# Kernel optimization log

Hardware: AMD Instinct MI355X
Metric: run time of the kernel (lower is better)

## Reference

```python
import jax, jax.numpy as jnp
import numpy as np
from jax import lax

NUM_MASK_PARAMS = 67  # 66 weights (64 feat + 2 coord channels) + 1 bias
NUM_GEN_PARAMS = 134


def _coord_maps(h, w, dtype):
    yy = jnp.broadcast_to(jnp.linspace(-1.0, 1.0, h, dtype=dtype)[:, None], (h, w))
    xx = jnp.broadcast_to(jnp.linspace(-1.0, 1.0, w, dtype=dtype)[None, :], (h, w))
    return xx, yy


def _dynamic_head(x_cat, p):
    # x_cat: [66, H, W]; p: [num_ins, 67] -> [num_ins, H, W]
    w = p[:, :NUM_MASK_PARAMS - 1]
    b = p[:, NUM_MASK_PARAMS - 1]
    return jnp.einsum('ic,chw->ihw', w, x_cat) + b[:, None, None]


def setup_inputs() -> dict:
    key = jax.random.key(0)
    ks = jax.random.split(key, 10)
    C, HM, WM, HH, WH, MB, HID = 256, 272, 480, 136, 240, 64, 64
    rn = lambda k, s, sc=1.0: jax.random.normal(k, s, dtype=jnp.float32) * sc
    return {
        'out0': rn(ks[0], (1, C, HM, WM)),
        'out1': rn(ks[1], (1, C, HH, WH)),
        'hm_w': rn(ks[2], (1, C), 0.05),
        'hm_b': jnp.zeros((1,), jnp.float32),
        'params_w': rn(ks[3], (NUM_GEN_PARAMS, C), 0.05),
        'params_b': rn(ks[4], (NUM_GEN_PARAMS,), 0.05),
        'mb_w': rn(ks[5], (MB, C, 3, 3), 0.05),
        'mb_b': jnp.zeros((MB,), jnp.float32),
        'mlp_w1': rn(ks[6], (HM, HID), 0.05),
        'mlp_b1': jnp.zeros((HID,), jnp.float32),
        'mlp_w2': rn(ks[7], (HID, 2), 0.05),
        'mlp_b2': jnp.zeros((2,), jnp.float32),
        'num_ins': 4,
    }


def reference(out0, out1, hm_w, hm_b, params_w, params_b, mb_w, mb_b,
              mlp_w1, mlp_b1, mlp_w2, mlp_b2, num_ins):
    h_mask, w_mask = out0.shape[2], out0.shape[3]
    h_hm, w_hm = out1.shape[2], out1.shape[3]

    # ctnet head: 1x1 convs on the stride-16 feature
    hm = jnp.einsum('kc,bchw->bkhw', hm_w, out1) + hm_b[None, :, None, None]
    params = jnp.einsum('kc,bchw->bkhw', params_w, out1) + params_b[None, :, None, None]
    hm = jnp.clip(jax.nn.sigmoid(hm), 1e-4, 1.0 - 1e-4)  # [1,1,h_hm,w_hm]
    # [1,134,h,w] -> [h*w, 134]
    params_flat = jnp.transpose(params[0], (1, 2, 0)).reshape(-1, NUM_GEN_PARAMS)

    # 3x3 maxpool NMS (stride 1, pad 1), keep only local peaks
    hmax = lax.reduce_window(hm, -jnp.inf, lax.max, (1, 1, 3, 3), (1, 1, 1, 1),
                             [(0, 0), (0, 0), (1, 1), (1, 1)])
    keep = (hmax == hm).astype(hm.dtype)
    heat_nms = (hm * keep).reshape(-1)

    scores, inds = lax.top_k(heat_nms, num_ins)

    # mask branch: 3x3 conv + relu on the stride-8 feature
    mask_branch = lax.conv_general_dilated(out0, mb_w, (1, 1), 'SAME',
                                           dimension_numbers=('NCHW', 'OIHW', 'NCHW'))
    mask_branch = jax.nn.relu(mask_branch + mb_b[None, :, None, None])  # [1,64,H,W]

    xx, yy = _coord_maps(h_mask, w_mask, mask_branch.dtype)
    x_cat = jnp.concatenate([mask_branch[0], xx[None], yy[None]], axis=0)  # [66,H,W]

    gen_params = params_flat[inds]  # [num_ins, 134]
    masks0 = _dynamic_head(x_cat, gen_params[:, :NUM_MASK_PARAMS])   # [num_ins,H,W]
    regs0 = _dynamic_head(x_cat, gen_params[:, NUM_MASK_PARAMS:])    # [num_ins,H,W]

    # row-wise vertical-range MLP over h_mask
    feat_range = jnp.transpose(masks0, (0, 2, 1))  # [num_ins, w_mask, h_mask]
    h1 = jax.nn.relu(feat_range @ mlp_w1 + mlp_b1)
    feat_range = h1 @ mlp_w2 + mlp_b2  # [num_ins, w_mask, 2]

    return scores, inds, regs0, masks0, feat_range
```

## Files before the change

kernel.cpp:

```cpp
#include <hip/hip_runtime.h>
#include <math.h>
#include <limits.h>

#define C_IN 256
#define HM_H 136
#define HM_W 240
#define HM_N (HM_H * HM_W)
#define MB   64
#define MH   272
#define MW   480
#define MN   (MH * MW)
#define NP   134
#define NI   4
#define HID  64

#define REG_OFF   8
#define MASK_OFF  (8 + NI * MN)
#define FEAT_OFF  (8 + 2 * NI * MN)

#define WS_HM   0
#define WS_CV   HM_N
#define WS_CI   (HM_N + 512)
#define WS_GP   (2 * HM_N)
#define WS_WT_F 65824

typedef float  f32x4  __attribute__((ext_vector_type(4)));
typedef short  bf16x8 __attribute__((ext_vector_type(8)));
typedef unsigned short u16x8 __attribute__((ext_vector_type(8)));

__device__ __forceinline__ unsigned short f2bf(float f) {
  unsigned int u = __float_as_uint(f);
  u += 0x7FFFu + ((u >> 16) & 1u);
  return (unsigned short)(u >> 16);
}
__device__ __forceinline__ float b2f(unsigned short h) {
  return __uint_as_float(((unsigned int)h) << 16);
}

__device__ __forceinline__ void glds16(const void* g, void* l) {
  __builtin_amdgcn_global_load_lds(
      (const __attribute__((address_space(1))) unsigned int*)g,
      (__attribute__((address_space(3))) unsigned int*)l, 16, 0, 0);
}

__global__ void k_prep(const float* __restrict__ mb_w, unsigned short* __restrict__ wt,
                       const float* __restrict__ out1, const float* __restrict__ hm_w,
                       const float* __restrict__ hm_b, float* __restrict__ ws_hm) {
  __shared__ float part[4][64];
  if (blockIdx.x < 576) {
    int idx = blockIdx.x * 256 + threadIdx.x;
    int j    = idx & 7;
    int lane = (idx >> 3) & 63;
    int nt   = (idx >> 9) & 3;
    int gt   = idx >> 11;
    int t    = gt % 9;
    int g    = gt / 9;
    int n = nt * 16 + (lane & 15);
    int c = g * 32 + (lane >> 4) * 8 + j;
    wt[idx] = f2bf(mb_w[(n * C_IN + c) * 9 + t]);
  } else {
    int b = blockIdx.x - 576, t = threadIdx.x;
    int cg = t >> 6, pl = t & 63;
    int p = b * 64 + pl;
    float s = 0.f;
    #pragma unroll 16
    for (int c = 0; c < 64; ++c)
      s += hm_w[cg * 64 + c] * out1[(cg * 64 + c) * HM_N + p];
    part[cg][pl] = s;
    __syncthreads();
    if (t < 64) {
      float tot = part[0][t] + part[1][t] + part[2][t] + part[3][t] + hm_b[0];
      float sig = 1.f / (1.f + expf(-tot));
      sig = fminf(fmaxf(sig, 1e-4f), 1.f - 1e-4f);
      ws_hm[b * 64 + t] = sig;
    }
  }
}

__device__ __forceinline__ bool better(float av, int ai, float bv, int bi) {
  return (av > bv) || (av == bv && ai < bi);
}

template<int NTHR>
__device__ void top4_tree(float* sv, int* si, int t) {
  for (int s = NTHR / 2; s >= 1; s >>= 1) {
    if (t < s) {
      float a[4], b[4]; int ai[4], bj[4];
      #pragma unroll
      for (int k = 0; k < 4; ++k) {
        a[k] = sv[t * 4 + k];        ai[k] = si[t * 4 + k];
        b[k] = sv[(t + s) * 4 + k];  bj[k] = si[(t + s) * 4 + k];
      }
      float ov[4]; int oi[4];
      int i = 0, j = 0;
      #pragma unroll
      for (int k = 0; k < 4; ++k) {
        if (better(a[i], ai[i], b[j], bj[j])) { ov[k] = a[i]; oi[k] = ai[i]; ++i; }
        else                                   { ov[k] = b[j]; oi[k] = bj[j]; ++j; }
      }
      #pragma unroll
      for (int k = 0; k < 4; ++k) { sv[t * 4 + k] = ov[k]; si[t * 4 + k] = oi[k]; }
    }
    __syncthreads();
  }
}

__global__ void k_nms_top(const float* __restrict__ ws_hm, float* __restrict__ candv,
                          int* __restrict__ candi) {
  __shared__ float sv[256 * 4];
  __shared__ int   si[256 * 4];
  int b = blockIdx.x, t = threadIdx.x;
  float v = -1.f; int idx = INT_MAX;
  if (t < 255) {
    int p = b * 255 + t;
    int y = p / HM_W, x = p - y * HM_W;
    float c = ws_hm[p], m = c;
    #pragma unroll
    for (int dy = -1; dy <= 1; ++dy)
      #pragma unroll
      for (int dx = -1; dx <= 1; ++dx) {
        int yy = y + dy, xx = x + dx;
        if (yy >= 0 && yy < HM_H && xx >= 0 && xx < HM_W)
          m = fmaxf(m, ws_hm[yy * HM_W + xx]);
      }
    v = (c == m) ? c : 0.f;
    idx = p;
  }
  sv[t * 4] = v; si[t * 4] = idx;
  #pragma unroll
  for (int k = 1; k < 4; ++k) { sv[t * 4 + k] = -1.f; si[t * 4 + k] = INT_MAX; }
  __syncthreads();
  top4_tree<256>(sv, si, t);
  if (t == 0) {
    #pragma unroll
    for (int k = 0; k < 4; ++k) { candv[b * 4 + k] = sv[k]; candi[b * 4 + k] = si[k]; }
  }
}

__global__ void k_gen(const float* __restrict__ candv, const int* __restrict__ candi,
                      const float* __restrict__ out1, const float* __restrict__ params_w,
                      const float* __restrict__ params_b, float* __restrict__ ws_gp,
                      float* __restrict__ d_out) {
  __shared__ float sv[128 * 4];
  __shared__ int   si[128 * 4];
  __shared__ float col[C_IN];
  int t = threadIdx.x, i = blockIdx.x;
  if (t < 128) {
    #pragma unroll
    for (int k = 0; k < 4; ++k) { sv[t * 4 + k] = candv[t * 4 + k]; si[t * 4 + k] = candi[t * 4 + k]; }
  }
  __syncthreads();
  top4_tree<128>(sv, si, t);
  if (i == 0 && t < 4) {
    d_out[t]     = sv[t];
    d_out[4 + t] = (float)si[t];
  }
  int p = si[i];
  col[t] = out1[t * HM_N + p];
  __syncthreads();
  if (t < NP) {
    float s = params_b[t];
    #pragma unroll 8
    for (int c = 0; c < C_IN; ++c) s += params_w[t * C_IN + c] * col[c];
    ws_gp[i * NP + t] = s;
  }
}

#define RP   36
#define BUFU (10 * RP * 32)
#define WOFF (2 * BUFU)

#define PIPE_BARRIER() do {                                   \
    __builtin_amdgcn_sched_barrier(0);                        \
    asm volatile("s_waitcnt lgkmcnt(0)" ::: "memory");        \
    __builtin_amdgcn_s_barrier();                             \
    __builtin_amdgcn_sched_barrier(0);                        \
  } while (0)

#define STAGE_W(G)                                                        \
  if (wv == 7 && (G) < 24) {                                              \
    const char* wsrc = (const char*)wt + (G) * 12288 + lane * 16;         \
    char* wdst = (char*)smem + 46080 + ((G) & 1) * 12288;                 \
    _Pragma("unroll")                                                     \
    for (int i_ = 0; i_ < 12; ++i_)                                       \
      glds16(wsrc + i_ * 1024, wdst + i_ * 1024);                         \
  }

#define TAPS3(P) {                                                        \
    const unsigned short* wl = smem + WOFF + (((g + (P)) & 1) * 6144)     \
                               + ce * 1024 + lane * 8;                    \
    _Pragma("unroll")                                                     \
    for (int tt = 0; tt < 3; ++tt) {                                      \
      bf16x8 bb0 = *(const bf16x8*)(wl + tt * 2048);                      \
      bf16x8 bb1 = *(const bf16x8*)(wl + tt * 2048 + 512);                \
      unsigned pk = lrdp[(P) * 3 + tt];                                   \
      const unsigned short* c0 = cur + (pk & 0xFFFFu);                    \
      const unsigned short* c1 = cur + (pk >> 16);                        \
      bf16x8 a0 = *(const bf16x8*)c0;                                     \
      bf16x8 a1 = *(const bf16x8*)(c0 + 512);                             \
      bf16x8 a2 = *(const bf16x8*)c1;                                     \
      bf16x8 a3 = *(const bf16x8*)(c1 + 512);                             \
      acc[0][0] = __builtin_amdgcn_mfma_f32_16x16x32_bf16(a0, bb0, acc[0][0], 0, 0, 0); \
      acc[0][1] = __builtin_amdgcn_mfma_f32_16x16x32_bf16(a0, bb1, acc[0][1], 0, 0, 0); \
      acc[1][0] = __builtin_amdgcn_mfma_f32_16x16x32_bf16(a1, bb0, acc[1][0], 0, 0, 0); \
      acc[1][1] = __builtin_amdgcn_mfma_f32_16x16x32_bf16(a1, bb1, acc[1][1], 0, 0, 0); \
      acc[2][0] = __builtin_amdgcn_mfma_f32_16x16x32_bf16(a2, bb0, acc[2][0], 0, 0, 0); \
      acc[2][1] = __builtin_amdgcn_mfma_f32_16x16x32_bf16(a2, bb1, acc[2][1], 0, 0, 0); \
      acc[3][0] = __builtin_amdgcn_mfma_f32_16x16x32_bf16(a3, bb0, acc[3][0], 0, 0, 0); \
      acc[3][1] = __builtin_amdgcn_mfma_f32_16x16x32_bf16(a3, bb1, acc[3][1], 0, 0, 0); \
    } }

__device__ __forceinline__ void stage_store8(unsigned short* buf, const f32x4* dq,
                                             bool gv, const int* lw, unsigned sm) {
  #pragma unroll
  for (int e = 0; e < 4; ++e) if ((sm >> e) & 1u) {
    u16x8 v;
    #pragma unroll
    for (int j = 0; j < 8; ++j) v[j] = f2bf(gv ? dq[j][e] : 0.f);
    *(u16x8*)(buf + lw[e]) = v;
  }
}

__global__ __launch_bounds__(512, 3) void k_conv_mfma(
    const float* __restrict__ out0, const unsigned short* __restrict__ wt,
    const float* __restrict__ mb_b, const float* __restrict__ ws_gp,
    float* __restrict__ d_out) {
  __shared__ unsigned short smem[2 * BUFU + 2 * 6144];

  int tid  = threadIdx.x;
  int lane = tid & 63;
  int wv   = tid >> 6;
  int n15  = lane & 15;
  int kq   = lane >> 4;
  int pg   = wv & 3;
  int ce   = wv >> 2;
  int gx0 = blockIdx.x * 32, gy0 = blockIdx.y * 8;

  bool act = tid < 400;
  int u    = act ? tid : 0;
  int co8  = u / 100;
  int rem  = u - co8 * 100;
  int row  = rem / 10;
  int qx   = rem - row * 10;
  int iy   = gy0 + row - 1;
  int ixq  = gx0 + 4 * qx - 4;
  bool gvld = act && (iy >= 0) && (iy < MH) && (ixq >= 0) && (ixq + 3 < MW);
  int goff  = gvld ? (co8 * 8 * MN + iy * MW + ixq) : 0;
  int lws[4]; unsigned smask = 0;
  #pragma unroll
  for (int e = 0; e < 4; ++e) {
    int sx = 4 * qx - 3 + e;
    bool sv = act && (sx >= 0) && (sx < RP);
    int pixw = row * RP + (sv ? sx : 0);
    int w2 = (pixw ^ (pixw >> 2)) & 3;
    int q  = (pixw ^ row) & 1;
    lws[e] = (pixw >> 1) * 64 + ((co8 ^ w2) << 4) + q * 8;
    if (sv) smask |= (1u << e);
  }

  unsigned lrdp[9];
  #pragma unroll
  for (int t = 0; t < 9; ++t) {
    int ty = t / 3, tx = t - ty * 3;
    int sr0 = pg * 2 + ty;
    int pix0 = sr0 * RP + n15 + tx;
    int w20 = (pix0 ^ (pix0 >> 2)) & 3;
    int q0  = (pix0 ^ sr0) & 1;
    unsigned o0 = (pix0 >> 1) * 64 + ((kq ^ w20) << 4) + q0 * 8;
    int sr1 = sr0 + 1;
    int pix1 = sr1 * RP + n15 + tx;
    int w21 = (pix1 ^ (pix1 >> 2)) & 3;
    int q1  = (pix1 ^ sr1) & 1;
    unsigned o1 = (pix1 >> 1) * 64 + ((kq ^ w21) << 4) + q1 * 8;
    lrdp[t] = o0 | (o1 << 16);
  }

  bool aload = (tid < 448);

  f32x4 dq[8];
  if (act) {
    const float* sp = out0 + goff;
    #pragma unroll
    for (int j = 0; j < 8; ++j) dq[j] = *(const f32x4*)(sp + j * MN);
  }
  stage_store8(smem, dq, gvld, lws, smask);
  __builtin_amdgcn_sched_barrier(0);
  if (act) {
    const float* sp = out0 + 32 * MN + goff;
    #pragma unroll
    for (int j = 0; j < 8; ++j) dq[j] = *(const f32x4*)(sp + j * MN);
  }
  STAGE_W(0);
  if (wv == 7) asm volatile("s_waitcnt vmcnt(0)" ::: "memory");
  PIPE_BARRIER();

  f32x4 acc[4][2];
  #pragma unroll
  for (int i = 0; i < 4; ++i)
    #pragma unroll
    for (int nt = 0; nt < 2; ++nt)
      acc[i][nt] = (f32x4){0.f, 0.f, 0.f, 0.f};

  #pragma unroll 1
  for (int g = 0; g < 8; ++g) {
    const unsigned short* cur = smem + (g & 1) * BUFU;
    unsigned short*       nxt = smem + ((g + 1) & 1) * BUFU;

    STAGE_W(3 * g + 1);
    if (g <= 6) stage_store8(nxt, dq, gvld, lws, smask);
    __builtin_amdgcn_sched_barrier(0);
    if (g <= 5 && act) {
      const float* sp = out0 + (g + 2) * (32 * MN) + goff;
      #pragma unroll
      for (int j = 0; j < 8; ++j) dq[j] = *(const f32x4*)(sp + j * MN);
    }
    __builtin_amdgcn_sched_barrier(0);
    TAPS3(0)
    if (wv == 7) asm volatile("s_waitcnt vmcnt(0)" ::: "memory");
    PIPE_BARRIER();

    STAGE_W(3 * g + 2);
    TAPS3(1)
    if (wv == 7) asm volatile("s_waitcnt vmcnt(0)" ::: "memory");
    PIPE_BARRIER();

    STAGE_W(3 * g + 3);
    TAPS3(2)
    if (wv == 7) asm volatile("s_waitcnt vmcnt(0)" ::: "memory");
    PIPE_BARRIER();
  }

  #define ES 66
  {
    float bias[2];
    #pragma unroll
    for (int nt = 0; nt < 2; ++nt) bias[nt] = mb_b[(ce * 2 + nt) * 16 + n15];
    #pragma unroll
    for (int i = 0; i < 4; ++i) {
      int mt = pg * 4 + i;
      int pbase = (mt >> 1) * 32 + (mt & 1) * 16;
      #pragma unroll
      for (int nt = 0; nt < 2; ++nt)
        #pragma unroll
        for (int reg = 0; reg < 4; ++reg) {
          float vv = fmaxf(acc[i][nt][reg] + bias[nt], 0.f);
          smem[(pbase + kq * 4 + reg) * ES + (ce * 2 + nt) * 16 + n15] = f2bf(vv);
        }
    }
  }
  __syncthreads();

  int p = tid & 255, hh = tid >> 8;
  int ob = hh * 32;
  float mres[4] = {0.f, 0.f, 0.f, 0.f};
  float rres[4] = {0.f, 0.f, 0.f, 0.f};
  #pragma unroll 8
  for (int o = 0; o < 32; ++o) {
    float v = b2f(smem[p * ES + ob + o]);
    #pragma unroll
    for (int i = 0; i < 4; ++i) {
      mres[i] += ws_gp[i * NP + ob + o] * v;
      rres[i] += ws_gp[i * NP + 67 + ob + o] * v;
    }
  }
  float* pf = (float*)smem + 8704;
  if (hh) {
    #pragma unroll
    for (int i = 0; i < 4; ++i) { pf[p * 8 + i] = mres[i]; pf[p * 8 + 4 + i] = rres[i]; }
  }
  __syncthreads();
  if (!hh) {
    int r = p >> 5, xcol = p & 31;
    int gy = gy0 + r, gx = gx0 + xcol;
    float xc = -1.f + (2.f / 479.f) * (float)gx;
    float yc = -1.f + (2.f / 271.f) * (float)gy;
    int pix = gy * MW + gx;
    #pragma unroll
    for (int i = 0; i < 4; ++i) {
      const float* gp = ws_gp + i * NP;
      d_out[MASK_OFF + i * MN + pix] = mres[i] + pf[p * 8 + i]     + gp[66]  + gp[64]  * xc + gp[65]  * yc;
      d_out[REG_OFF  + i * MN + pix] = rres[i] + pf[p * 8 + 4 + i] + gp[133] + gp[131] * xc + gp[132] * yc;
    }
  }
  (void)aload;
}

__global__ void k_mlp(const float* __restrict__ masks0, const float* __restrict__ w1,
                      const float* __restrict__ b1, const float* __restrict__ w2,
                      const float* __restrict__ b2, float* __restrict__ d_out) {
  int blk = blockIdx.x;
  int i = blk / MW;
  int w = blk - i * MW;
  int k = threadIdx.x;
  const float* mcol = masks0 + i * MN + w;
  float s = b1[k];
  #pragma unroll 4
  for (int h = 0; h < MH; ++h) s += mcol[h * MW] * w1[h * HID + k];
  s = fmaxf(s, 0.f);
  float o0 = s * w2[k * 2 + 0];
  float o1 = s * w2[k * 2 + 1];
  #pragma unroll
  for (int off = 32; off >= 1; off >>= 1) {
    o0 += __shfl_down(o0, off);
    o1 += __shfl_down(o1, off);
  }
  if (k == 0) {
    d_out[FEAT_OFF + blk * 2 + 0] = o0 + b2[0];
    d_out[FEAT_OFF + blk * 2 + 1] = o1 + b2[1];
  }
}

extern "C" void kernel_launch(void* const* d_in, const int* in_sizes, int n_in,
                              void* d_out, int out_size, void* d_ws, size_t ws_size,
                              hipStream_t stream) {
  const float* out0     = (const float*)d_in[0];
  const float* out1     = (const float*)d_in[1];
  const float* hm_w     = (const float*)d_in[2];
  const float* hm_b     = (const float*)d_in[3];
  const float* params_w = (const float*)d_in[4];
  const float* params_b = (const float*)d_in[5];
  const float* mb_w     = (const float*)d_in[6];
  const float* mb_b     = (const float*)d_in[7];
  const float* mlp_w1   = (const float*)d_in[8];
  const float* mlp_b1   = (const float*)d_in[9];
  const float* mlp_w2   = (const float*)d_in[10];
  const float* mlp_b2   = (const float*)d_in[11];

  float* ws      = (float*)d_ws;
  float* ws_hm   = ws + WS_HM;
  float* candv   = ws + WS_CV;
  int*   candi   = (int*)(ws + WS_CI);
  float* ws_gp   = ws + WS_GP;
  unsigned short* ws_wt = (unsigned short*)(ws + WS_WT_F);
  float* out     = (float*)d_out;

  k_prep<<<1086, 256, 0, stream>>>(mb_w, ws_wt, out1, hm_w, hm_b, ws_hm);
  k_nms_top<<<128, 256, 0, stream>>>(ws_hm, candv, candi);
  k_gen<<<NI, 256, 0, stream>>>(candv, candi, out1, params_w, params_b, ws_gp, out);
  dim3 gconv(MW / 32, MH / 8);
  k_conv_mfma<<<gconv, 512, 0, stream>>>(out0, ws_wt, mb_b, ws_gp, out);
  k_mlp<<<NI * MW, 64, 0, stream>>>(out + MASK_OFF, mlp_w1, mlp_b1, mlp_w2, mlp_b2, out);
}
```

Before: 328.1 us.

## Enlarge conv MFMA tile to 16 rows with all 64 output channels per wave

The 3x3 conv kernel now processes a 32x16 pixel tile per block instead of 32x8. Each wave covers two output rows across all 64 output channels (4x4 accumulator tiles) instead of splitting the channels across wave groups. This cuts redundant halo loads and reuses each A fragment across more MFMAs. Weight staging becomes a triple buffer, and each input channel group is split into two 16-channel halves staged across the tap phases with partial vmcnt waits. In exchange it uses more registers and LDS, drops occupancy from 3 to 2 blocks per CU, halves the grid, and loops the epilogue over two pixel halves.

```diff
diff --git a/kernel.cpp b/kernel.cpp
--- a/kernel.cpp
+++ b/kernel.cpp
@@ -166,8 +166,9 @@
   }
 }
 
+#define SR   18
 #define RP   36
-#define BUFU (10 * RP * 32)
+#define BUFU (SR * RP * 32)
 #define WOFF (2 * BUFU)
 
 #define PIPE_BARRIER() do {                                   \
@@ -177,22 +178,25 @@
     __builtin_amdgcn_sched_barrier(0);                        \
   } while (0)
 
-#define STAGE_W(G)                                                        \
+#define STAGE_W3(G, B)                                                    \
   if (wv == 7 && (G) < 24) {                                              \
     const char* wsrc = (const char*)wt + (G) * 12288 + lane * 16;         \
-    char* wdst = (char*)smem + 46080 + ((G) & 1) * 12288;                 \
+    char* wdst = (char*)smem + 2 * WOFF + (B) * 12288;                    \
     _Pragma("unroll")                                                     \
     for (int i_ = 0; i_ < 12; ++i_)                                       \
       glds16(wsrc + i_ * 1024, wdst + i_ * 1024);                         \
   }
 
+#define MFMA16(A, B, C) __builtin_amdgcn_mfma_f32_16x16x32_bf16(A, B, C, 0, 0, 0)
+
 #define TAPS3(P) {                                                        \
-    const unsigned short* wl = smem + WOFF + (((g + (P)) & 1) * 6144)     \
-                               + ce * 1024 + lane * 8;                    \
+    const unsigned short* wl = smem + WOFF + (P) * 6144 + lane * 8;       \
     _Pragma("unroll")                                                     \
     for (int tt = 0; tt < 3; ++tt) {                                      \
       bf16x8 bb0 = *(const bf16x8*)(wl + tt * 2048);                      \
       bf16x8 bb1 = *(const bf16x8*)(wl + tt * 2048 + 512);                \
+      bf16x8 bb2 = *(const bf16x8*)(wl + tt * 2048 + 1024);               \
+      bf16x8 bb3 = *(const bf16x8*)(wl + tt * 2048 + 1536);               \
       unsigned pk = lrdp[(P) * 3 + tt];                                   \
       const unsigned short* c0 = cur + (pk & 0xFFFFu);                    \
       const unsigned short* c1 = cur + (pk >> 16);                        \
@@ -200,14 +204,22 @@
       bf16x8 a1 = *(const bf16x8*)(c0 + 512);                             \
       bf16x8 a2 = *(const bf16x8*)c1;                                     \
       bf16x8 a3 = *(const bf16x8*)(c1 + 512);                             \
-      acc[0][0] = __builtin_amdgcn_mfma_f32_16x16x32_bf16(a0, bb0, acc[0][0], 0, 0, 0); \
-      acc[0][1] = __builtin_amdgcn_mfma_f32_16x16x32_bf16(a0, bb1, acc[0][1], 0, 0, 0); \
-      acc[1][0] = __builtin_amdgcn_mfma_f32_16x16x32_bf16(a1, bb0, acc[1][0], 0, 0, 0); \
-      acc[1][1] = __builtin_amdgcn_mfma_f32_16x16x32_bf16(a1, bb1, acc[1][1], 0, 0, 0); \
-      acc[2][0] = __builtin_amdgcn_mfma_f32_16x16x32_bf16(a2, bb0, acc[2][0], 0, 0, 0); \
-      acc[2][1] = __builtin_amdgcn_mfma_f32_16x16x32_bf16(a2, bb1, acc[2][1], 0, 0, 0); \
-      acc[3][0] = __builtin_amdgcn_mfma_f32_16x16x32_bf16(a3, bb0, acc[3][0], 0, 0, 0); \
-      acc[3][1] = __builtin_amdgcn_mfma_f32_16x16x32_bf16(a3, bb1, acc[3][1], 0, 0, 0); \
+      acc[0][0] = MFMA16(a0, bb0, acc[0][0]);                             \
+      acc[0][1] = MFMA16(a0, bb1, acc[0][1]);                             \
+      acc[0][2] = MFMA16(a0, bb2, acc[0][2]);                             \
+      acc[0][3] = MFMA16(a0, bb3, acc[0][3]);                             \
+      acc[1][0] = MFMA16(a1, bb0, acc[1][0]);                             \
+      acc[1][1] = MFMA16(a1, bb1, acc[1][1]);                             \
+      acc[1][2] = MFMA16(a1, bb2, acc[1][2]);                             \
+      acc[1][3] = MFMA16(a1, bb3, acc[1][3]);                             \
+      acc[2][0] = MFMA16(a2, bb0, acc[2][0]);                             \
+      acc[2][1] = MFMA16(a2, bb1, acc[2][1]);                             \
+      acc[2][2] = MFMA16(a2, bb2, acc[2][2]);                             \
+      acc[2][3] = MFMA16(a2, bb3, acc[2][3]);                             \
+      acc[3][0] = MFMA16(a3, bb0, acc[3][0]);                             \
+      acc[3][1] = MFMA16(a3, bb1, acc[3][1]);                             \
+      acc[3][2] = MFMA16(a3, bb2, acc[3][2]);                             \
+      acc[3][3] = MFMA16(a3, bb3, acc[3][3]);                             \
     } }
 
 __device__ __forceinline__ void stage_store8(unsigned short* buf, const f32x4* dq,
@@ -221,40 +233,38 @@
   }
 }
 
-__global__ __launch_bounds__(512, 3) void k_conv_mfma(
+__global__ __launch_bounds__(512, 2) void k_conv_mfma(
     const float* __restrict__ out0, const unsigned short* __restrict__ wt,
     const float* __restrict__ mb_b, const float* __restrict__ ws_gp,
     float* __restrict__ d_out) {
-  __shared__ unsigned short smem[2 * BUFU + 2 * 6144];
+  __shared__ unsigned short smem[2 * BUFU + 3 * 6144];
 
   int tid  = threadIdx.x;
   int lane = tid & 63;
   int wv   = tid >> 6;
   int n15  = lane & 15;
   int kq   = lane >> 4;
-  int pg   = wv & 3;
-  int ce   = wv >> 2;
-  int gx0 = blockIdx.x * 32, gy0 = blockIdx.y * 8;
-
-  bool act = tid < 400;
-  int u    = act ? tid : 0;
-  int co8  = u / 100;
-  int rem  = u - co8 * 100;
+  int gx0 = blockIdx.x * 32, gy0 = blockIdx.y * 16;
+
+  bool ustage = tid < 360;
+  int u    = ustage ? tid : 0;
+  int co8  = u / 180;
+  int rem  = u - co8 * 180;
   int row  = rem / 10;
   int qx   = rem - row * 10;
   int iy   = gy0 + row - 1;
   int ixq  = gx0 + 4 * qx - 4;
-  bool gvld = act && (iy >= 0) && (iy < MH) && (ixq >= 0) && (ixq + 3 < MW);
-  int goff  = gvld ? (co8 * 8 * MN + iy * MW + ixq) : 0;
-  int lws[4]; unsigned smask = 0;
+  bool gvld = ustage && (iy >= 0) && (iy < MH) && (ixq >= 0) && (ixq + 3 < MW);
+  int goffA = gvld ? (co8 * 8 * MN + iy * MW + ixq) : 0;
+  int lwsA[4]; unsigned smask = 0;
   #pragma unroll
   for (int e = 0; e < 4; ++e) {
     int sx = 4 * qx - 3 + e;
-    bool sv = act && (sx >= 0) && (sx < RP);
+    bool sv = ustage && (sx >= 0) && (sx < RP);
     int pixw = row * RP + (sv ? sx : 0);
     int w2 = (pixw ^ (pixw >> 2)) & 3;
     int q  = (pixw ^ row) & 1;
-    lws[e] = (pixw >> 1) * 64 + ((co8 ^ w2) << 4) + q * 8;
+    lwsA[e] = (pixw >> 1) * 64 + ((co8 ^ w2) << 4) + q * 8;
     if (sv) smask |= (1u << e);
   }
 
@@ -262,7 +272,7 @@
   #pragma unroll
   for (int t = 0; t < 9; ++t) {
     int ty = t / 3, tx = t - ty * 3;
-    int sr0 = pg * 2 + ty;
+    int sr0 = 2 * wv + ty;
     int pix0 = sr0 * RP + n15 + tx;
     int w20 = (pix0 ^ (pix0 >> 2)) & 3;
     int q0  = (pix0 ^ sr0) & 1;
@@ -275,76 +285,102 @@
     lrdp[t] = o0 | (o1 << 16);
   }
 
-  bool aload = (tid < 448);
-
-  f32x4 dq[8];
-  if (act) {
-    const float* sp = out0 + goff;
-    #pragma unroll
-    for (int j = 0; j < 8; ++j) dq[j] = *(const f32x4*)(sp + j * MN);
-  }
-  stage_store8(smem, dq, gvld, lws, smask);
+  {
+    f32x4 dq[8];
+    if (ustage) {
+      const float* sp = out0 + goffA;
+      #pragma unroll
+      for (int j = 0; j < 8; ++j) dq[j] = *(const f32x4*)(sp + j * MN);
+    }
+    stage_store8(smem, dq, gvld, lwsA, smask);
+    if (ustage) {
+      const float* sp = out0 + goffA + 16 * MN;
+      #pragma unroll
+      for (int j = 0; j < 8; ++j) dq[j] = *(const f32x4*)(sp + j * MN);
+    }
+    {
+      int lwsB[4];
+      #pragma unroll
+      for (int e = 0; e < 4; ++e) lwsB[e] = lwsA[e] ^ 32;
+      stage_store8(smem, dq, gvld, lwsB, smask);
+    }
+  }
   __builtin_amdgcn_sched_barrier(0);
-  if (act) {
-    const float* sp = out0 + 32 * MN + goff;
-    #pragma unroll
-    for (int j = 0; j < 8; ++j) dq[j] = *(const f32x4*)(sp + j * MN);
-  }
-  STAGE_W(0);
-  if (wv == 7) asm volatile("s_waitcnt vmcnt(0)" ::: "memory");
+  STAGE_W3(0, 0);
+  STAGE_W3(1, 1);
+  if (wv == 7) asm volatile("s_waitcnt vmcnt(12)" ::: "memory");
   PIPE_BARRIER();
 
-  f32x4 acc[4][2];
+  f32x4 acc[4][4];
   #pragma unroll
   for (int i = 0; i < 4; ++i)
     #pragma unroll
-    for (int nt = 0; nt < 2; ++nt)
+    for (int nt = 0; nt < 4; ++nt)
       acc[i][nt] = (f32x4){0.f, 0.f, 0.f, 0.f};
 
   #pragma unroll 1
   for (int g = 0; g < 8; ++g) {
     const unsigned short* cur = smem + (g & 1) * BUFU;
     unsigned short*       nxt = smem + ((g + 1) & 1) * BUFU;
-
-    STAGE_W(3 * g + 1);
-    if (g <= 6) stage_store8(nxt, dq, gvld, lws, smask);
-    __builtin_amdgcn_sched_barrier(0);
-    if (g <= 5 && act) {
-      const float* sp = out0 + (g + 2) * (32 * MN) + goff;
+    const float*          src = out0 + (g + 1) * (32 * MN);
+    f32x4 dq[8];
+
+    STAGE_W3(3 * g + 2, 2);
+    if (g < 7 && ustage) {
+      const float* sp = src + goffA;
       #pragma unroll
       for (int j = 0; j < 8; ++j) dq[j] = *(const f32x4*)(sp + j * MN);
     }
     __builtin_amdgcn_sched_barrier(0);
     TAPS3(0)
-    if (wv == 7) asm volatile("s_waitcnt vmcnt(0)" ::: "memory");
+    if (wv == 7) asm volatile("s_waitcnt vmcnt(12)" ::: "memory");
     PIPE_BARRIER();
 
-    STAGE_W(3 * g + 2);
+    STAGE_W3(3 * g + 3, 0);
+    if (g < 7) stage_store8(nxt, dq, gvld, lwsA, smask);
+    if (g < 7 && ustage) {
+      const float* sp = src + goffA + 16 * MN;
+      #pragma unroll
+      for (int j = 0; j < 8; ++j) dq[j] = *(const f32x4*)(sp + j * MN);
+    }
+    __builtin_amdgcn_sched_barrier(0);
     TAPS3(1)
-    if (wv == 7) asm volatile("s_waitcnt vmcnt(0)" ::: "memory");
+    if (wv == 7) {
+      if (g == 7) asm volatile("s_waitcnt vmcnt(0)" ::: "memory");
+      else        asm volatile("s_waitcnt vmcnt(12)" ::: "memory");
+    }
     PIPE_BARRIER();
 
-    STAGE_W(3 * g + 3);
+    STAGE_W3(3 * g + 4, 1);
+    if (g < 7) {
+      int lwsB[4];
+      #pragma unroll
+      for (int e = 0; e < 4; ++e) lwsB[e] = lwsA[e] ^ 32;
+      stage_store8(nxt, dq, gvld, lwsB, smask);
+    }
+    __builtin_amdgcn_sched_barrier(0);
     TAPS3(2)
-    if (wv == 7) asm volatile("s_waitcnt vmcnt(0)" ::: "memory");
+    if (wv == 7) {
+      if (g == 7) asm volatile("s_waitcnt vmcnt(0)" ::: "memory");
+      else        asm volatile("s_waitcnt vmcnt(12)" ::: "memory");
+    }
     PIPE_BARRIER();
   }
 
   #define ES 66
   {
-    float bias[2];
-    #pragma unroll
-    for (int nt = 0; nt < 2; ++nt) bias[nt] = mb_b[(ce * 2 + nt) * 16 + n15];
+    float bias[4];
+    #pragma unroll
+    for (int nt = 0; nt < 4; ++nt) bias[nt] = mb_b[nt * 16 + n15];
     #pragma unroll
     for (int i = 0; i < 4; ++i) {
-      int mt = pg * 4 + i;
-      int pbase = (mt >> 1) * 32 + (mt & 1) * 16;
-      #pragma unroll
-      for (int nt = 0; nt < 2; ++nt)
+      int pbase = (2 * wv + (i >> 1)) * 32 + (i & 1) * 16;
+      #pragma unroll
+      for (int nt = 0; nt < 4; ++nt)
         #pragma unroll
         for (int reg = 0; reg < 4; ++reg) {
           float vv = fmaxf(acc[i][nt][reg] + bias[nt], 0.f);
-          smem[(pbase + kq * 4 + reg) * ES + (ce * 2 + nt) * 16 + n15] = f2bf(vv);
+          smem[(pbase + kq * 4 + reg) * ES + nt * 16 + n15] = f2bf(vv);
         }
     }
   }
@@ -352,37 +388,41 @@
 
   int p = tid & 255, hh = tid >> 8;
   int ob = hh * 32;
-  float mres[4] = {0.f, 0.f, 0.f, 0.f};
-  float rres[4] = {0.f, 0.f, 0.f, 0.f};
-  #pragma unroll 8
-  for (int o = 0; o < 32; ++o) {
-    float v = b2f(smem[p * ES + ob + o]);
-    #pragma unroll
-    for (int i = 0; i < 4; ++i) {
-      mres[i] += ws_gp[i * NP + ob + o] * v;
-      rres[i] += ws_gp[i * NP + 67 + ob + o] * v;
-    }
-  }
-  float* pf = (float*)smem + 8704;
-  if (hh) {
-    #pragma unroll
-    for (int i = 0; i < 4; ++i) { pf[p * 8 + i] = mres[i]; pf[p * 8 + 4 + i] = rres[i]; }
-  }
-  __syncthreads();
-  if (!hh) {
-    int r = p >> 5, xcol = p & 31;
-    int gy = gy0 + r, gx = gx0 + xcol;
-    float xc = -1.f + (2.f / 479.f) * (float)gx;
-    float yc = -1.f + (2.f / 271.f) * (float)gy;
-    int pix = gy * MW + gx;
-    #pragma unroll
-    for (int i = 0; i < 4; ++i) {
-      const float* gp = ws_gp + i * NP;
-      d_out[MASK_OFF + i * MN + pix] = mres[i] + pf[p * 8 + i]     + gp[66]  + gp[64]  * xc + gp[65]  * yc;
-      d_out[REG_OFF  + i * MN + pix] = rres[i] + pf[p * 8 + 4 + i] + gp[133] + gp[131] * xc + gp[132] * yc;
-    }
-  }
-  (void)aload;
+  float* pf = (float*)smem + 16896;
+  #pragma unroll 1
+  for (int ps = 0; ps < 2; ++ps) {
+    int pixel = ps * 256 + p;
+    float mres[4] = {0.f, 0.f, 0.f, 0.f};
+    float rres[4] = {0.f, 0.f, 0.f, 0.f};
+    #pragma unroll 8
+    for (int o = 0; o < 32; ++o) {
+      float v = b2f(smem[pixel * ES + ob + o]);
+      #pragma unroll
+      for (int i = 0; i < 4; ++i) {
+        mres[i] += ws_gp[i * NP + ob + o] * v;
+        rres[i] += ws_gp[i * NP + 67 + ob + o] * v;
+      }
+    }
+    if (hh) {
+      #pragma unroll
+      for (int i = 0; i < 4; ++i) { pf[p * 8 + i] = mres[i]; pf[p * 8 + 4 + i] = rres[i]; }
+    }
+    __syncthreads();
+    if (!hh) {
+      int r = pixel >> 5, xcol = pixel & 31;
+      int gy = gy0 + r, gx = gx0 + xcol;
+      float xc = -1.f + (2.f / 479.f) * (float)gx;
+      float yc = -1.f + (2.f / 271.f) * (float)gy;
+      int pix = gy * MW + gx;
+      #pragma unroll
+      for (int i = 0; i < 4; ++i) {
+        const float* gp = ws_gp + i * NP;
+        d_out[MASK_OFF + i * MN + pix] = mres[i] + pf[p * 8 + i]     + gp[66]  + gp[64]  * xc + gp[65]  * yc;
+        d_out[REG_OFF  + i * MN + pix] = rres[i] + pf[p * 8 + 4 + i] + gp[133] + gp[131] * xc + gp[132] * yc;
+      }
+    }
+    __syncthreads();
+  }
 }
 
 __global__ void k_mlp(const float* __restrict__ masks0, const float* __restrict__ w1,
@@ -437,7 +477,7 @@
   k_prep<<<1086, 256, 0, stream>>>(mb_w, ws_wt, out1, hm_w, hm_b, ws_hm);
   k_nms_top<<<128, 256, 0, stream>>>(ws_hm, candv, candi);
   k_gen<<<NI, 256, 0, stream>>>(candv, candi, out1, params_w, params_b, ws_gp, out);
-  dim3 gconv(MW / 32, MH / 8);
+  dim3 gconv(MW / 32, MH / 16);
   k_conv_mfma<<<gconv, 512, 0, stream>>>(out0, ws_wt, mb_b, ws_gp, out);
   k_mlp<<<NI * MW, 64, 0, stream>>>(out + MASK_OFF, mlp_w1, mlp_b1, mlp_w2, mlp_b2, out);
 }
```

After: 311.6 us. 5.0% less time.

## Remap conv MFMA tiles per wave, add XCD-aware block order, stage MLP column in LDS

Applied to the files above, without the earlier changes.

The conv kernel's wave decomposition changes from 4 pixel groups × 2 channel halves to one wave per output row, each computing 2×16 pixels × all 64 channels (acc[2][4]). A-fragment LDS reads per tap drop and B-fragment reads rise. The weight buffer parity now uses 3*g+P, fixing staging alternation. The grid becomes 1D with an XCD-aware remap so neighbouring tiles share an L2, and launch bounds rise to 4 blocks per CU. The MLP kernel stages the strided mask column in shared memory once before the dot product, trading an extra barrier for fewer redundant global loads.

```diff
diff --git a/kernel.cpp b/kernel.cpp
--- a/kernel.cpp
+++ b/kernel.cpp
@@ -166,8 +166,9 @@
   }
 }
 
+#define SR   10
 #define RP   36
-#define BUFU (10 * RP * 32)
+#define BUFU (SR * RP * 32)
 #define WOFF (2 * BUFU)
 
 #define PIPE_BARRIER() do {                                   \
@@ -186,28 +187,28 @@
       glds16(wsrc + i_ * 1024, wdst + i_ * 1024);                         \
   }
 
+#define MFMA16(A, B, C) __builtin_amdgcn_mfma_f32_16x16x32_bf16(A, B, C, 0, 0, 0)
+
 #define TAPS3(P) {                                                        \
-    const unsigned short* wl = smem + WOFF + (((g + (P)) & 1) * 6144)     \
-                               + ce * 1024 + lane * 8;                    \
+    const unsigned short* wl = smem + WOFF + (((3 * g + (P)) & 1) * 6144) \
+                               + lane * 8;                                \
     _Pragma("unroll")                                                     \
     for (int tt = 0; tt < 3; ++tt) {                                      \
       bf16x8 bb0 = *(const bf16x8*)(wl + tt * 2048);                      \
       bf16x8 bb1 = *(const bf16x8*)(wl + tt * 2048 + 512);                \
-      unsigned pk = lrdp[(P) * 3 + tt];                                   \
-      const unsigned short* c0 = cur + (pk & 0xFFFFu);                    \
-      const unsigned short* c1 = cur + (pk >> 16);                        \
+      bf16x8 bb2 = *(const bf16x8*)(wl + tt * 2048 + 1024);               \
+      bf16x8 bb3 = *(const bf16x8*)(wl + tt * 2048 + 1536);               \
+      const unsigned short* c0 = cur + lrdp[(P) * 3 + tt];                \
       bf16x8 a0 = *(const bf16x8*)c0;                                     \
       bf16x8 a1 = *(const bf16x8*)(c0 + 512);                             \
-      bf16x8 a2 = *(const bf16x8*)c1;                                     \
-      bf16x8 a3 = *(const bf16x8*)(c1 + 512);                             \
-      acc[0][0] = __builtin_amdgcn_mfma_f32_16x16x32_bf16(a0, bb0, acc[0][0], 0, 0, 0); \
-      acc[0][1] = __builtin_amdgcn_mfma_f32_16x16x32_bf16(a0, bb1, acc[0][1], 0, 0, 0); \
-      acc[1][0] = __builtin_amdgcn_mfma_f32_16x16x32_bf16(a1, bb0, acc[1][0], 0, 0, 0); \
-      acc[1][1] = __builtin_amdgcn_mfma_f32_16x16x32_bf16(a1, bb1, acc[1][1], 0, 0, 0); \
-      acc[2][0] = __builtin_amdgcn_mfma_f32_16x16x32_bf16(a2, bb0, acc[2][0], 0, 0, 0); \
-      acc[2][1] = __builtin_amdgcn_mfma_f32_16x16x32_bf16(a2, bb1, acc[2][1], 0, 0, 0); \
-      acc[3][0] = __builtin_amdgcn_mfma_f32_16x16x32_bf16(a3, bb0, acc[3][0], 0, 0, 0); \
-      acc[3][1] = __builtin_amdgcn_mfma_f32_16x16x32_bf16(a3, bb1, acc[3][1], 0, 0, 0); \
+      acc[0][0] = MFMA16(a0, bb0, acc[0][0]);                             \
+      acc[0][1] = MFMA16(a0, bb1, acc[0][1]);                             \
+      acc[0][2] = MFMA16(a0, bb2, acc[0][2]);                             \
+      acc[0][3] = MFMA16(a0, bb3, acc[0][3]);                             \
+      acc[1][0] = MFMA16(a1, bb0, acc[1][0]);                             \
+      acc[1][1] = MFMA16(a1, bb1, acc[1][1]);                             \
+      acc[1][2] = MFMA16(a1, bb2, acc[1][2]);                             \
+      acc[1][3] = MFMA16(a1, bb3, acc[1][3]);                             \
     } }
 
 __device__ __forceinline__ void stage_store8(unsigned short* buf, const f32x4* dq,
@@ -221,7 +222,7 @@
   }
 }
 
-__global__ __launch_bounds__(512, 3) void k_conv_mfma(
+__global__ __launch_bounds__(512, 4) void k_conv_mfma(
     const float* __restrict__ out0, const unsigned short* __restrict__ wt,
     const float* __restrict__ mb_b, const float* __restrict__ ws_gp,
     float* __restrict__ d_out) {
@@ -232,25 +233,28 @@
   int wv   = tid >> 6;
   int n15  = lane & 15;
   int kq   = lane >> 4;
-  int pg   = wv & 3;
-  int ce   = wv >> 2;
-  int gx0 = blockIdx.x * 32, gy0 = blockIdx.y * 8;
-
-  bool act = tid < 400;
-  int u    = act ? tid : 0;
+
+  int orig = blockIdx.x;
+  int xcd  = orig & 7, pos = orig >> 3;
+  int wgid = (xcd < 6) ? (xcd * 64 + pos) : (384 + (xcd - 6) * 63 + pos);
+  int bx = wgid / 34, by = wgid - bx * 34;
+  int gx0 = bx * 32, gy0 = by * 8;
+
+  bool ustage = tid < 400;
+  int u    = ustage ? tid : 0;
   int co8  = u / 100;
   int rem  = u - co8 * 100;
   int row  = rem / 10;
   int qx   = rem - row * 10;
   int iy   = gy0 + row - 1;
   int ixq  = gx0 + 4 * qx - 4;
-  bool gvld = act && (iy >= 0) && (iy < MH) && (ixq >= 0) && (ixq + 3 < MW);
+  bool gvld = ustage && (iy >= 0) && (iy < MH) && (ixq >= 0) && (ixq + 3 < MW);
   int goff  = gvld ? (co8 * 8 * MN + iy * MW + ixq) : 0;
   int lws[4]; unsigned smask = 0;
   #pragma unroll
   for (int e = 0; e < 4; ++e) {
     int sx = 4 * qx - 3 + e;
-    bool sv = act && (sx >= 0) && (sx < RP);
+    bool sv = ustage && (sx >= 0) && (sx < RP);
     int pixw = row * RP + (sv ? sx : 0);
     int w2 = (pixw ^ (pixw >> 2)) & 3;
     int q  = (pixw ^ row) & 1;
@@ -262,43 +266,36 @@
   #pragma unroll
   for (int t = 0; t < 9; ++t) {
     int ty = t / 3, tx = t - ty * 3;
-    int sr0 = pg * 2 + ty;
-    int pix0 = sr0 * RP + n15 + tx;
-    int w20 = (pix0 ^ (pix0 >> 2)) & 3;
-    int q0  = (pix0 ^ sr0) & 1;
-    unsigned o0 = (pix0 >> 1) * 64 + ((kq ^ w20) << 4) + q0 * 8;
-    int sr1 = sr0 + 1;
-    int pix1 = sr1 * RP + n15 + tx;
-    int w21 = (pix1 ^ (pix1 >> 2)) & 3;
-    int q1  = (pix1 ^ sr1) & 1;
-    unsigned o1 = (pix1 >> 1) * 64 + ((kq ^ w21) << 4) + q1 * 8;
-    lrdp[t] = o0 | (o1 << 16);
-  }
-
-  bool aload = (tid < 448);
+    int sr = wv + ty;
+    int pix = sr * RP + n15 + tx;
+    int w2 = (pix ^ (pix >> 2)) & 3;
+    int q  = (pix ^ sr) & 1;
+    lrdp[t] = (pix >> 1) * 64 + ((kq ^ w2) << 4) + q * 8;
+  }
 
   f32x4 dq[8];
-  if (act) {
+  if (ustage) {
     const float* sp = out0 + goff;
     #pragma unroll
     for (int j = 0; j < 8; ++j) dq[j] = *(const f32x4*)(sp + j * MN);
   }
   stage_store8(smem, dq, gvld, lws, smask);
   __builtin_amdgcn_sched_barrier(0);
-  if (act) {
+  if (ustage) {
     const float* sp = out0 + 32 * MN + goff;
     #pragma unroll
     for (int j = 0; j < 8; ++j) dq[j] = *(const f32x4*)(sp + j * MN);
   }
+  __builtin_amdgcn_sched_barrier(0);
   STAGE_W(0);
   if (wv == 7) asm volatile("s_waitcnt vmcnt(0)" ::: "memory");
   PIPE_BARRIER();
 
-  f32x4 acc[4][2];
-  #pragma unroll
-  for (int i = 0; i < 4; ++i)
-    #pragma unroll
-    for (int nt = 0; nt < 2; ++nt)
+  f32x4 acc[2][4];
+  #pragma unroll
+  for (int i = 0; i < 2; ++i)
+    #pragma unroll
+    for (int nt = 0; nt < 4; ++nt)
       acc[i][nt] = (f32x4){0.f, 0.f, 0.f, 0.f};
 
   #pragma unroll 1
@@ -307,9 +304,9 @@
     unsigned short*       nxt = smem + ((g + 1) & 1) * BUFU;
 
     STAGE_W(3 * g + 1);
-    if (g <= 6) stage_store8(nxt, dq, gvld, lws, smask);
+    if (g < 7) stage_store8(nxt, dq, gvld, lws, smask);
     __builtin_amdgcn_sched_barrier(0);
-    if (g <= 5 && act) {
+    if (g < 6 && ustage) {
       const float* sp = out0 + (g + 2) * (32 * MN) + goff;
       #pragma unroll
       for (int j = 0; j < 8; ++j) dq[j] = *(const f32x4*)(sp + j * MN);
@@ -332,19 +329,18 @@
 
   #define ES 66
   {
-    float bias[2];
-    #pragma unroll
-    for (int nt = 0; nt < 2; ++nt) bias[nt] = mb_b[(ce * 2 + nt) * 16 + n15];
-    #pragma unroll
-    for (int i = 0; i < 4; ++i) {
-      int mt = pg * 4 + i;
-      int pbase = (mt >> 1) * 32 + (mt & 1) * 16;
-      #pragma unroll
-      for (int nt = 0; nt < 2; ++nt)
+    float bias[4];
+    #pragma unroll
+    for (int nt = 0; nt < 4; ++nt) bias[nt] = mb_b[nt * 16 + n15];
+    #pragma unroll
+    for (int i = 0; i < 2; ++i) {
+      int pbase = wv * 32 + i * 16;
+      #pragma unroll
+      for (int nt = 0; nt < 4; ++nt)
         #pragma unroll
         for (int reg = 0; reg < 4; ++reg) {
           float vv = fmaxf(acc[i][nt][reg] + bias[nt], 0.f);
-          smem[(pbase + kq * 4 + reg) * ES + (ce * 2 + nt) * 16 + n15] = f2bf(vv);
+          smem[(pbase + kq * 4 + reg) * ES + nt * 16 + n15] = f2bf(vv);
         }
     }
   }
@@ -382,20 +378,22 @@
       d_out[REG_OFF  + i * MN + pix] = rres[i] + pf[p * 8 + 4 + i] + gp[133] + gp[131] * xc + gp[132] * yc;
     }
   }
-  (void)aload;
 }
 
 __global__ void k_mlp(const float* __restrict__ masks0, const float* __restrict__ w1,
                       const float* __restrict__ b1, const float* __restrict__ w2,
                       const float* __restrict__ b2, float* __restrict__ d_out) {
+  __shared__ float ms[MH];
   int blk = blockIdx.x;
   int i = blk / MW;
   int w = blk - i * MW;
   int k = threadIdx.x;
   const float* mcol = masks0 + i * MN + w;
+  for (int h = k; h < MH; h += 64) ms[h] = mcol[h * MW];
+  __syncthreads();
   float s = b1[k];
-  #pragma unroll 4
-  for (int h = 0; h < MH; ++h) s += mcol[h * MW] * w1[h * HID + k];
+  #pragma unroll 8
+  for (int h = 0; h < MH; ++h) s += ms[h] * w1[h * HID + k];
   s = fmaxf(s, 0.f);
   float o0 = s * w2[k * 2 + 0];
   float o1 = s * w2[k * 2 + 1];
@@ -437,7 +435,6 @@
   k_prep<<<1086, 256, 0, stream>>>(mb_w, ws_wt, out1, hm_w, hm_b, ws_hm);
   k_nms_top<<<128, 256, 0, stream>>>(ws_hm, candv, candi);
   k_gen<<<NI, 256, 0, stream>>>(candv, candi, out1, params_w, params_b, ws_gp, out);
-  dim3 gconv(MW / 32, MH / 8);
-  k_conv_mfma<<<gconv, 512, 0, stream>>>(out0, ws_wt, mb_b, ws_gp, out);
+  k_conv_mfma<<<510, 512, 0, stream>>>(out0, ws_wt, mb_b, ws_gp, out);
   k_mlp<<<NI * MW, 64, 0, stream>>>(out + MASK_OFF, mlp_w1, mlp_b1, mlp_w2, mlp_b2, out);
 }
```

Result: faster. 319.5 us (-2.6%).
